# Kernel tuning notes

Hardware: AMD Instinct MI355X
Metric: run time of the kernel (lower is better)

Reference implementation:

```python
import jax, jax.numpy as jnp
import numpy as np

B, S, D, H, HD = 8, 1374, 384, 6, 64
NUM_PATCHES = 1369  # (518 // 14) ** 2
NUM_PREFIX = 5      # 1 cls + 4 registers


def setup_inputs() -> dict:
    key = jax.random.key(0)
    ks = jax.random.split(key, 10)
    init = 0.02  # truncated_normal(0.02) approximated by scaled normal
    x = jax.random.normal(ks[0], (B, S, D), jnp.float32)
    wq = jax.random.truncated_normal(ks[1], -2.0, 2.0, (D, H, HD), jnp.float32) * init
    wk = jax.random.truncated_normal(ks[2], -2.0, 2.0, (D, H, HD), jnp.float32) * init
    wv = jax.random.truncated_normal(ks[3], -2.0, 2.0, (D, H, HD), jnp.float32) * init
    wo = jax.random.truncated_normal(ks[4], -2.0, 2.0, (H, HD, D), jnp.float32) * init
    bq = jnp.zeros((H, HD), jnp.float32)
    bk = jnp.zeros((H, HD), jnp.float32)
    bv = jnp.zeros((H, HD), jnp.float32)
    bo = jnp.zeros((D,), jnp.float32)
    keep_patch_indices = jax.random.randint(ks[5], (B, NUM_PATCHES), 0, NUM_PATCHES).astype(jnp.int64)
    return {"x": x, "wq": wq, "bq": bq, "wk": wk, "bk": bk, "wv": wv, "bv": bv,
            "wo": wo, "bo": bo, "keep_patch_indices": keep_patch_indices, "k_patches": 685}


def reference(x, wq, bq, wk, bk, wv, bv, wo, bo, keep_patch_indices, k_patches):
    # q/k/v projections: DenseGeneral to (heads, head_dim)
    q = jnp.einsum('bsd,dhe->bshe', x, wq) + bq
    k = jnp.einsum('bsd,dhe->bshe', x, wk) + bk
    v = jnp.einsum('bsd,dhe->bshe', x, wv) + bv

    z = jnp.einsum('bqhd,bkhd->bhqk', q / (HD ** 0.5), k)  # [B,H,S,S]
    attn_logits = z  # saved BEFORE masking (used by 'mse' criterion)

    # dynamic scatter mask: patch columns >= k_patches get -inf
    num_selected = keep_patch_indices.shape[1]
    patch_idx = jnp.arange(num_selected)
    indices_to_mask = jnp.where(patch_idx >= k_patches, patch_idx, num_selected) + NUM_PREFIX
    # out-of-bounds indices (== num_selected + NUM_PREFIX) are dropped by JAX scatter semantics
    z = z.at[:, :, :, indices_to_mask].set(-jnp.inf)

    attn_map = jax.nn.softmax(z, axis=-1)
    zo = jnp.einsum('bhqk,bkhd->bqhd', attn_map, v)
    output = jnp.einsum('bqhd,hdo->bqo', zo, wo) + bo  # wo contracts (heads, head_dim)

    # attn_aggregate = ['cls_token','reg_token','patch_token'], zoom_map_criterion='mse'
    am = attn_logits.mean(axis=1)  # mean over heads -> [B,S,S]
    aggs = jnp.stack([
        am[:, 0:1, :].mean(axis=1),      # cls token
        am[:, 1:5, :].mean(axis=1),      # register tokens
        am[:, 5:1374, :].mean(axis=1),   # patch tokens
    ], axis=1)                            # [B,3,S]
    attn_agg = aggs.mean(axis=1)          # [B,S]
    return output, attn_agg
```

## Files before the change

### kernel.cpp

```cpp
#include <hip/hip_runtime.h>
#include <stdint.h>

#define BB 8
#define SS 1374
#define DD 384
#define HH 6
#define HDIM 64
#define MROWS (BB*SS)
#define NPFX 5
#define SPAD 1376

typedef __attribute__((ext_vector_type(8))) short bf16x8;
typedef __attribute__((ext_vector_type(4))) float f32x4;
typedef __attribute__((ext_vector_type(2))) unsigned int u32x2;
typedef __attribute__((ext_vector_type(4))) unsigned int u32x4;
typedef u32x4 __attribute__((aligned(4))) u32x4_u;

__device__ __forceinline__ unsigned short f2bf(float f){
  union { float f; unsigned int u; } v; v.f = f;
  return (unsigned short)((v.u + 0x7FFFu + ((v.u >> 16) & 1u)) >> 16);
}
__device__ __forceinline__ float bf2f(unsigned short b){
  union { float f; unsigned int u; } v; v.u = ((unsigned int)b) << 16; return v.f;
}
__device__ __forceinline__ unsigned int pk_bf16(float a, float b){
#if __has_builtin(__builtin_amdgcn_cvt_pk_bf16_f32)
  typedef __attribute__((ext_vector_type(2))) __bf16 bfv2;
  bfv2 p = __builtin_amdgcn_cvt_pk_bf16_f32(a, b);
  union { bfv2 v; unsigned int u; } c; c.v = p; return c.u;
#else
  return (unsigned int)f2bf(a) | ((unsigned int)f2bf(b) << 16);
#endif
}

__global__ void k_prep_x(const float* __restrict__ x, unsigned short* __restrict__ xb,
                         float* __restrict__ xbar){
  int b = blockIdx.x / 43, ch = blockIdx.x % 43;
  int d = threadIdx.x;
  int s0 = ch*32, s1 = s0 + 32; if (s1 > SS) s1 = SS;
  float acc = 0.f;
  for (int s = s0; s < s1; ++s){
    float v = x[((size_t)b*SS + s)*DD + d];
    float w = (s == 0) ? (1.f/3.f) : (s < 5) ? (1.f/12.f) : (1.f/4107.f);
    acc += w * v;
    xb[((size_t)b*SS + s)*DD + d] = f2bf(v);
  }
  atomicAdd(&xbar[b*DD + d], acc);
}

__global__ void k_conv_w(const float* __restrict__ wq, const float* __restrict__ wk,
                         const float* __restrict__ wv, const float* __restrict__ wo,
                         unsigned short* __restrict__ wbT, unsigned short* __restrict__ woT){
  int i = blockIdx.x*blockDim.x + threadIdx.x;
  if (i < 1152*384){
    int n = i / 384, d = i % 384;
    const float* w = (n < 384) ? wq : (n < 768) ? wk : wv;
    wbT[i] = f2bf(w[(size_t)d*384 + (n % 384)]);
  } else if (i < 1152*384 + 384*384){
    int j = i - 1152*384;
    int n = j / 384, k = j % 384;
    woT[j] = f2bf(wo[(size_t)k*384 + n]);
  }
}

__global__ void k_qbar(const float* __restrict__ xbar, const float* __restrict__ wq,
                       const float* __restrict__ bq, float* __restrict__ qbar){
  __shared__ float xs[DD];
  int b = blockIdx.x, t = threadIdx.x;
  xs[t] = xbar[b*DD + t];
  __syncthreads();
  float acc = bq[t];
  for (int d = 0; d < DD; ++d) acc += xs[d]*wq[(size_t)d*384 + t];
  qbar[b*384 + t] = acc;
}

__global__ void k_agg(const float* __restrict__ qbar, const unsigned short* __restrict__ kg,
                      float* __restrict__ out_agg){
  __shared__ float qs[384];
  int b = blockIdx.x / 6, sb = blockIdx.x % 6;
  int t = threadIdx.x;
  for (int i = t; i < 384; i += 256) qs[i] = qbar[b*384 + i];
  __syncthreads();
  int s = sb*256 + t;
  if (s >= SS) return;
  float acc = 0.f;
  for (int h = 0; h < HH; ++h){
    const unsigned short* kr = kg + (((size_t)(b*HH + h))*SS + s)*64;
    const float* qh = qs + h*64;
    for (int c = 0; c < 8; ++c){
      u32x4 v = *(const u32x4*)(kr + c*8);
      #pragma unroll
      for (int j = 0; j < 4; ++j){
        unsigned int u = v[j];
        acc += qh[c*8 + 2*j]     * bf2f((unsigned short)(u & 0xFFFFu));
        acc += qh[c*8 + 2*j + 1] * bf2f((unsigned short)(u >> 16));
      }
    }
  }
  out_agg[b*SS + s] = acc * (1.f/48.f);
}

template<int MODE>
__global__ __launch_bounds__(256) void k_gemm(
    const unsigned short* __restrict__ A, const unsigned short* __restrict__ Bt,
    const float* __restrict__ b0, const float* __restrict__ b1, const float* __restrict__ b2,
    unsigned short* __restrict__ qg, unsigned short* __restrict__ kgp,
    unsigned short* __restrict__ vt, float* __restrict__ out)
{
  int mt = blockIdx.x % 86, nt = blockIdx.x / 86;
  const int t = threadIdx.x;
  const int w = t >> 6, lane = t & 63, quad = lane >> 4, l16 = lane & 15;
  const int wm = w >> 1, wn = w & 1;
  constexpr int SMEM_SH = (MODE==0) ? 13824 : 17408;
  __shared__ unsigned short smem[SMEM_SH];
  unsigned short* As = smem;
  unsigned short* Bs = smem + 9216;
  f32x4 acc[4][2];
  #pragma unroll
  for (int i=0;i<4;i++){ acc[i][0] = (f32x4){0,0,0,0}; acc[i][1] = (f32x4){0,0,0,0}; }
  const int m0 = mt*128, n0 = nt*64;

  const int ar = t >> 1, akb = (t & 1) * 32;
  int ga = m0 + ar; if (ga > MROWS-1) ga = MROWS-1;
  const unsigned short* ap = A + (size_t)ga*384 + akb;
  const int br = t >> 2, bkb = (t & 3) * 16;
  const unsigned short* bp = Bt + (size_t)(n0 + br)*384 + bkb;

  u32x4 ra[4], rb[2];
  #pragma unroll
  for (int i=0;i<4;i++) ra[i] = *(const u32x4*)(ap + i*8);
  rb[0] = *(const u32x4*)(bp); rb[1] = *(const u32x4*)(bp + 8);

  for (int kc = 0; kc < 6; ++kc){
    __syncthreads();
    #pragma unroll
    for (int i=0;i<4;i++) *(u32x4*)(As + ar*72 + akb + i*8) = ra[i];
    *(u32x4*)(Bs + br*72 + bkb)     = rb[0];
    *(u32x4*)(Bs + br*72 + bkb + 8) = rb[1];
    __syncthreads();
    if (kc + 1 < 6){
      int kn = (kc+1)*64;
      #pragma unroll
      for (int i=0;i<4;i++) ra[i] = *(const u32x4*)(ap + kn + i*8);
      rb[0] = *(const u32x4*)(bp + kn); rb[1] = *(const u32x4*)(bp + kn + 8);
    }
    #pragma unroll
    for (int kh = 0; kh < 2; ++kh){
      bf16x8 af[4], bfr[2];
      #pragma unroll
      for (int rf = 0; rf < 4; ++rf)
        af[rf] = *(const bf16x8*)(As + (wm*64 + rf*16 + l16)*72 + kh*32 + quad*8);
      #pragma unroll
      for (int cf = 0; cf < 2; ++cf)
        bfr[cf] = *(const bf16x8*)(Bs + (wn*32 + cf*16 + l16)*72 + kh*32 + quad*8);
      #pragma unroll
      for (int rf = 0; rf < 4; ++rf)
        #pragma unroll
        for (int cf = 0; cf < 2; ++cf)
          acc[rf][cf] = __builtin_amdgcn_mfma_f32_16x16x32_bf16(af[rf], bfr[cf], acc[rf][cf], 0,0,0);
    }
  }

  const int b0r = m0 / SS, s0r = m0 % SS;
  __syncthreads();
  if (MODE == 1){
    float* CsF = (float*)smem;
    #pragma unroll
    for (int cf = 0; cf < 2; ++cf){
      int e = wn*32 + cf*16 + l16;
      float bias = b0[n0 + e];
      #pragma unroll
      for (int rf = 0; rf < 4; ++rf){
        int rr = wm*64 + rf*16 + quad*4;
        #pragma unroll
        for (int r4 = 0; r4 < 4; ++r4)
          CsF[(rr + r4)*68 + e] = acc[rf][cf][r4] + bias;
      }
    }
    __syncthreads();
    #pragma unroll
    for (int p = 0; p < 8; ++p){
      int r = p*16 + (t >> 4), c = t & 15;
      int rr = m0 + r;
      if (rr < MROWS){
        f32x4 v = *(const f32x4*)(CsF + r*68 + c*4);
        *(f32x4*)(out + (size_t)rr*384 + n0 + c*4) = v;
      }
    }
  } else {
    const int mat = nt / 6, h = nt - mat*6;
    const float* bvp = (mat==0) ? b0 : (mat==1) ? b1 : b2;
    const float vsc = (mat==0) ? 0.125f : 1.f;
    if (mat < 2){
      unsigned short* Cs = As;
      unsigned short* dst = (mat==0) ? qg : kgp;
      #pragma unroll
      for (int cf = 0; cf < 2; ++cf){
        int e = wn*32 + cf*16 + l16;
        float bias = bvp[h*64 + e];
        #pragma unroll
        for (int rf = 0; rf < 4; ++rf){
          int rr = wm*64 + rf*16 + quad*4;
          #pragma unroll
          for (int r4 = 0; r4 < 4; ++r4)
            Cs[(rr + r4)*72 + e] = f2bf((acc[rf][cf][r4] + bias)*vsc);
        }
      }
      __syncthreads();
      #pragma unroll
      for (int p = 0; p < 4; ++p){
        int r = p*32 + (t >> 3), c = t & 7;
        int rr = m0 + r;
        if (rr < MROWS){
          int s = s0r + r, bb = b0r;
          if (s >= SS){ s -= SS; ++bb; }
          u32x4 v = *(const u32x4*)(Cs + r*72 + c*8);
          *(u32x4*)(dst + (((size_t)(bb*HH + h))*SS + s)*64 + c*8) = v;
        }
      }
    } else {
      unsigned short* CsV = As;
      #pragma unroll
      for (int cf = 0; cf < 2; ++cf){
        int e = wn*32 + cf*16 + l16;
        float bias = bvp[h*64 + e];
        #pragma unroll
        for (int rf = 0; rf < 4; ++rf){
          int rr = wm*64 + rf*16 + quad*4;
          #pragma unroll
          for (int p = 0; p < 2; ++p)
            *(unsigned int*)(CsV + e*136 + rr + p*2) =
                pk_bf16(acc[rf][cf][p*2] + bias, acc[rf][cf][p*2+1] + bias);
        }
      }
      __syncthreads();
      const bool nowrap = (s0r + 127 < SS) && (m0 + 127 < MROWS);
      if (nowrap){
        int e = t >> 2;
        unsigned short* vrow = vt + ((size_t)(b0r*HH + h)*64 + e)*SPAD + s0r;
        #pragma unroll
        for (int i = 0; i < 4; ++i){
          int c = (t & 3)*4 + i;
          u32x4 v = *(const u32x4*)(CsV + e*136 + c*8);
          *(u32x4_u*)(vrow + c*8) = v;
        }
      } else {
        for (int idx = t; idx < 64*64; idx += 256){
          int e = idx >> 6, sp = (idx & 63)*2;
          int rr = m0 + sp;
          if (rr < MROWS){
            int s = s0r + sp, bb = b0r;
            if (s >= SS){ s -= SS; ++bb; }
            *(unsigned int*)(vt + ((size_t)(bb*HH + h)*64 + e)*SPAD + s) =
                *(const unsigned int*)(CsV + e*136 + sp);
          }
        }
      }
    }
  }
}

#define KSTR 72
__global__ __launch_bounds__(128) void k_attn(
    const unsigned short* __restrict__ qg, const unsigned short* __restrict__ kg,
    const unsigned short* __restrict__ vt, unsigned short* __restrict__ zo,
    const int* __restrict__ kpat)
{
  const int QB = 43;
  int qb = blockIdx.x % QB, bh = blockIdx.x / QB;
  int t = threadIdx.x, w = t >> 6, lane = t & 63, quad = lane >> 4, l16 = lane & 15;
  int SK = NPFX + kpat[0]; if (SK > SS) SK = SS; if (SK < 1) SK = 1;
  int niter = (SK + 63) >> 6;
  __shared__ unsigned short Ks[64*KSTR];
  __shared__ unsigned short Vs[64*KSTR];
  __shared__ unsigned short Ps[2][16*KSTR];
  unsigned short* Pw = &Ps[w][0];
  int q0 = qb*32 + w*16;
  bf16x8 aq[2];
  {
    int qrow = q0 + l16; if (qrow > SS-1) qrow = SS-1;
    const unsigned short* p = qg + ((size_t)bh*SS + qrow)*64;
    aq[0] = *(const bf16x8*)(p + quad*8);
    aq[1] = *(const bf16x8*)(p + 32 + quad*8);
  }
  f32x4 o[4];
  #pragma unroll
  for (int i=0;i<4;i++) o[i] = (f32x4){0.f,0.f,0.f,0.f};
  float rsum[4] = {0.f,0.f,0.f,0.f};

  const int srow = t >> 1, shalf = (t & 1)*32;
  const unsigned short* kbase = kg + ((size_t)bh*SS)*64;
  const unsigned short* vbase = vt + ((size_t)bh*64)*SPAD;
  u32x4 rk[4], rv[4];
  #pragma unroll
  for (int i=0;i<4;i++){
    rk[i] = *(const u32x4*)(kbase + (size_t)srow*64 + shalf + i*8);
    rv[i] = *(const u32x4*)(vbase + (size_t)srow*SPAD + shalf + i*8);
  }

  for (int it = 0; it < niter; ++it){
    int k0 = it*64;
    __syncthreads();
    #pragma unroll
    for (int i=0;i<4;i++){
      *(u32x4*)(Ks + srow*KSTR + shalf + i*8) = rk[i];
      *(u32x4*)(Vs + srow*KSTR + shalf + i*8) = rv[i];
    }
    __syncthreads();
    if (it + 1 < niter){
      int kn = k0 + 64;
      #pragma unroll
      for (int i=0;i<4;i++){
        rk[i] = *(const u32x4*)(kbase + (size_t)(kn + srow)*64 + shalf + i*8);
        rv[i] = *(const u32x4*)(vbase + (size_t)srow*SPAD + kn + shalf + i*8);
      }
    }
    bool tail = (k0 + 64 > SK);
    #pragma unroll
    for (int ks = 0; ks < 2; ++ks){
      float pp[2][4];
      #pragma unroll
      for (int ns = 0; ns < 2; ++ns){
        f32x4 zf = (f32x4){0.f,0.f,0.f,0.f};
        #pragma unroll
        for (int ec = 0; ec < 2; ++ec){
          bf16x8 bkf = *(const bf16x8*)(Ks + (ks*32 + 2*l16 + ns)*KSTR + ec*32 + quad*8);
          zf = __builtin_amdgcn_mfma_f32_16x16x32_bf16(aq[ec], bkf, zf, 0,0,0);
        }
        bool valid = !tail || (k0 + ks*32 + 2*l16 + ns) < SK;
        #pragma unroll
        for (int rg = 0; rg < 4; ++rg) pp[ns][rg] = valid ? __expf(zf[rg]) : 0.f;
      }
      #pragma unroll
      for (int rg = 0; rg < 4; ++rg){
        rsum[rg] += pp[0][rg] + pp[1][rg];
        *(unsigned int*)(Pw + (quad*4 + rg)*KSTR + ks*32 + 2*l16) =
            pk_bf16(pp[0][rg], pp[1][rg]);
      }
    }
    #pragma unroll
    for (int kc = 0; kc < 2; ++kc){
      bf16x8 ap = *(const bf16x8*)(Pw + l16*KSTR + kc*32 + quad*8);
      #pragma unroll
      for (int nc = 0; nc < 4; ++nc){
        bf16x8 vf = *(const bf16x8*)(Vs + (nc*16 + l16)*KSTR + kc*32 + quad*8);
        o[nc] = __builtin_amdgcn_mfma_f32_16x16x32_bf16(ap, vf, o[nc], 0,0,0);
      }
    }
  }
  int b = bh / HH, h = bh - (bh/HH)*HH;
  #pragma unroll
  for (int rg = 0; rg < 4; ++rg){
    float s = rsum[rg];
    #pragma unroll
    for (int off = 8; off >= 1; off >>= 1) s += __shfl_xor(s, off);
    int q = q0 + quad*4 + rg;
    if (q >= SS) continue;
    float inv = 1.f / s;
    unsigned short* dst = zo + ((size_t)b*SS + q)*384 + h*64;
    #pragma unroll
    for (int nc = 0; nc < 4; ++nc) dst[nc*16 + l16] = f2bf(o[nc][rg]*inv);
  }
}

extern "C" void kernel_launch(void* const* d_in, const int* in_sizes, int n_in,
                              void* d_out, int out_size, void* d_ws, size_t ws_size,
                              hipStream_t stream){
  const float* x  = (const float*)d_in[0];
  const float* wq = (const float*)d_in[1];
  const float* bq = (const float*)d_in[2];
  const float* wk = (const float*)d_in[3];
  const float* bk = (const float*)d_in[4];
  const float* wv = (const float*)d_in[5];
  const float* bv = (const float*)d_in[6];
  const float* wo = (const float*)d_in[7];
  const float* bo = (const float*)d_in[8];
  const int* kpat = (const int*)d_in[10];
  float* out = (float*)d_out;
  float* out_agg = out + (size_t)MROWS*DD;

  char* ws = (char*)d_ws;
  unsigned short* xb  = (unsigned short*)(ws);
  unsigned short* wbT = (unsigned short*)(ws +  8441856);
  unsigned short* woT = (unsigned short*)(ws +  9326592);
  unsigned short* qg  = (unsigned short*)(ws +  9621504);
  unsigned short* kg  = (unsigned short*)(ws + 18063360);
  unsigned short* vt  = (unsigned short*)(ws + 26505216);
  unsigned short* zo  = (unsigned short*)(ws + 34959360);
  float* xbar         = (float*)(ws + 43401216);
  float* qbar         = (float*)(ws + 43413504);
  (void)in_sizes; (void)n_in; (void)out_size; (void)ws_size;

  hipMemsetAsync(xbar, 0, BB*DD*sizeof(float), stream);
  k_prep_x<<<BB*43, DD, 0, stream>>>(x, xb, xbar);
  k_conv_w<<<((1152*384 + 384*384) + 255)/256, 256, 0, stream>>>(wq, wk, wv, wo, wbT, woT);
  k_qbar<<<BB, DD, 0, stream>>>(xbar, wq, bq, qbar);
  k_gemm<0><<<86*18, 256, 0, stream>>>(xb, wbT, bq, bk, bv, qg, kg, vt, nullptr);
  k_attn<<<48*43, 128, 0, stream>>>(qg, kg, vt, zo, kpat);
  k_agg<<<BB*6, 256, 0, stream>>>(qbar, kg, out_agg);
  k_gemm<1><<<86*6, 256, 0, stream>>>(zo, woT, bo, nullptr, nullptr, nullptr, nullptr, nullptr, out);
}
```

Before: 190.5 us.

## Skip dead V projection tiles and load K/V fragments directly in attention

The QKV GEMM now returns early for V-column tiles whose rows lie entirely in key positions that the mask excludes, so it never computes V values attention does not read. The attention kernel doubles the query rows per warp to 32, halving the grid. It drops the shared-memory K/V staging and its barriers, loading MFMA operand fragments straight from global memory with a register prefetch of the next K block. This reduces LDS traffic and synchronisation at the cost of uncoalesced fragment loads and higher register pressure.

```diff
diff --git a/kernel.cpp b/kernel.cpp
--- a/kernel.cpp
+++ b/kernel.cpp
@@ -105,12 +105,22 @@
     const unsigned short* __restrict__ A, const unsigned short* __restrict__ Bt,
     const float* __restrict__ b0, const float* __restrict__ b1, const float* __restrict__ b2,
     unsigned short* __restrict__ qg, unsigned short* __restrict__ kgp,
-    unsigned short* __restrict__ vt, float* __restrict__ out)
+    unsigned short* __restrict__ vt, float* __restrict__ out,
+    const int* __restrict__ kpat)
 {
   int mt = blockIdx.x % 86, nt = blockIdx.x / 86;
   const int t = threadIdx.x;
   const int w = t >> 6, lane = t & 63, quad = lane >> 4, l16 = lane & 15;
   const int wm = w >> 1, wn = w & 1;
+  const int m0 = mt*128, n0 = nt*64;
+
+  if (MODE == 0 && nt >= 12){
+    int s0r_ = m0 % SS;
+    int SKv = NPFX + kpat[0]; if (SKv > SS) SKv = SS; if (SKv < 1) SKv = 1;
+    int lo = (SKv + 63) & ~63;
+    if (s0r_ >= lo && s0r_ + 127 < SS) return;
+  }
+
   constexpr int SMEM_SH = (MODE==0) ? 13824 : 17408;
   __shared__ unsigned short smem[SMEM_SH];
   unsigned short* As = smem;
@@ -118,7 +128,6 @@
   f32x4 acc[4][2];
   #pragma unroll
   for (int i=0;i<4;i++){ acc[i][0] = (f32x4){0,0,0,0}; acc[i][1] = (f32x4){0,0,0,0}; }
-  const int m0 = mt*128, n0 = nt*64;
 
   const int ar = t >> 1, akb = (t & 1) * 32;
   int ga = m0 + ar; if (ga > MROWS-1) ga = MROWS-1;
@@ -260,107 +269,121 @@
   }
 }
 
-#define KSTR 72
+#define PSTR 80
 __global__ __launch_bounds__(128) void k_attn(
     const unsigned short* __restrict__ qg, const unsigned short* __restrict__ kg,
     const unsigned short* __restrict__ vt, unsigned short* __restrict__ zo,
     const int* __restrict__ kpat)
 {
-  const int QB = 43;
-  int qb = blockIdx.x % QB, bh = blockIdx.x / QB;
+  const int NQB = 22;
+  int qb = blockIdx.x % NQB, bh = blockIdx.x / NQB;
   int t = threadIdx.x, w = t >> 6, lane = t & 63, quad = lane >> 4, l16 = lane & 15;
   int SK = NPFX + kpat[0]; if (SK > SS) SK = SS; if (SK < 1) SK = 1;
   int niter = (SK + 63) >> 6;
-  __shared__ unsigned short Ks[64*KSTR];
-  __shared__ unsigned short Vs[64*KSTR];
-  __shared__ unsigned short Ps[2][16*KSTR];
+  __shared__ unsigned short Ps[2][32*PSTR];
   unsigned short* Pw = &Ps[w][0];
-  int q0 = qb*32 + w*16;
-  bf16x8 aq[2];
-  {
-    int qrow = q0 + l16; if (qrow > SS-1) qrow = SS-1;
+  int q0 = qb*64 + w*32;
+
+  bf16x8 aq[2][2];
+  #pragma unroll
+  for (int rt = 0; rt < 2; ++rt){
+    int qrow = q0 + rt*16 + l16; if (qrow > SS-1) qrow = SS-1;
     const unsigned short* p = qg + ((size_t)bh*SS + qrow)*64;
-    aq[0] = *(const bf16x8*)(p + quad*8);
-    aq[1] = *(const bf16x8*)(p + 32 + quad*8);
-  }
-  f32x4 o[4];
-  #pragma unroll
-  for (int i=0;i<4;i++) o[i] = (f32x4){0.f,0.f,0.f,0.f};
-  float rsum[4] = {0.f,0.f,0.f,0.f};
-
-  const int srow = t >> 1, shalf = (t & 1)*32;
+    aq[rt][0] = *(const bf16x8*)(p + quad*8);
+    aq[rt][1] = *(const bf16x8*)(p + 32 + quad*8);
+  }
+  f32x4 o[2][4];
+  float rsum[2][4];
+  #pragma unroll
+  for (int rt=0;rt<2;++rt){
+    #pragma unroll
+    for (int i=0;i<4;i++){ o[rt][i] = (f32x4){0.f,0.f,0.f,0.f}; rsum[rt][i] = 0.f; }
+  }
   const unsigned short* kbase = kg + ((size_t)bh*SS)*64;
   const unsigned short* vbase = vt + ((size_t)bh*64)*SPAD;
-  u32x4 rk[4], rv[4];
-  #pragma unroll
-  for (int i=0;i<4;i++){
-    rk[i] = *(const u32x4*)(kbase + (size_t)srow*64 + shalf + i*8);
-    rv[i] = *(const u32x4*)(vbase + (size_t)srow*SPAD + shalf + i*8);
-  }
+
+  bf16x8 kf[2][2][2];
+  #pragma unroll
+  for (int ks=0; ks<2; ++ks)
+    #pragma unroll
+    for (int ns=0; ns<2; ++ns){
+      const unsigned short* kp = kbase + (size_t)(ks*32 + 2*l16 + ns)*64;
+      kf[ks][ns][0] = *(const bf16x8*)(kp + quad*8);
+      kf[ks][ns][1] = *(const bf16x8*)(kp + 32 + quad*8);
+    }
 
   for (int it = 0; it < niter; ++it){
     int k0 = it*64;
-    __syncthreads();
-    #pragma unroll
-    for (int i=0;i<4;i++){
-      *(u32x4*)(Ks + srow*KSTR + shalf + i*8) = rk[i];
-      *(u32x4*)(Vs + srow*KSTR + shalf + i*8) = rv[i];
-    }
-    __syncthreads();
+    bool tail = (k0 + 64 > SK);
+    bf16x8 vf[2][4];
+    #pragma unroll
+    for (int kc=0;kc<2;++kc)
+      #pragma unroll
+      for (int nc=0;nc<4;++nc)
+        vf[kc][nc] = *(const bf16x8*)(vbase + (size_t)(nc*16 + l16)*SPAD + k0 + kc*32 + quad*8);
+
+    #pragma unroll
+    for (int ks=0;ks<2;++ks){
+      f32x4 zf[2][2];
+      #pragma unroll
+      for (int rt=0;rt<2;++rt)
+        #pragma unroll
+        for (int ns=0;ns<2;++ns){
+          f32x4 z = (f32x4){0.f,0.f,0.f,0.f};
+          z = __builtin_amdgcn_mfma_f32_16x16x32_bf16(aq[rt][0], kf[ks][ns][0], z, 0,0,0);
+          z = __builtin_amdgcn_mfma_f32_16x16x32_bf16(aq[rt][1], kf[ks][ns][1], z, 0,0,0);
+          zf[rt][ns] = z;
+        }
+      bool v0 = !tail || (k0 + ks*32 + 2*l16)     < SK;
+      bool v1 = !tail || (k0 + ks*32 + 2*l16 + 1) < SK;
+      #pragma unroll
+      for (int rt=0;rt<2;++rt){
+        #pragma unroll
+        for (int rg=0;rg<4;++rg){
+          float p0 = v0 ? __expf(zf[rt][0][rg]) : 0.f;
+          float p1 = v1 ? __expf(zf[rt][1][rg]) : 0.f;
+          rsum[rt][rg] += p0 + p1;
+          *(unsigned int*)(Pw + (rt*16 + quad*4 + rg)*PSTR + ks*32 + 2*l16) = pk_bf16(p0, p1);
+        }
+      }
+    }
     if (it + 1 < niter){
       int kn = k0 + 64;
       #pragma unroll
-      for (int i=0;i<4;i++){
-        rk[i] = *(const u32x4*)(kbase + (size_t)(kn + srow)*64 + shalf + i*8);
-        rv[i] = *(const u32x4*)(vbase + (size_t)srow*SPAD + kn + shalf + i*8);
-      }
-    }
-    bool tail = (k0 + 64 > SK);
-    #pragma unroll
-    for (int ks = 0; ks < 2; ++ks){
-      float pp[2][4];
-      #pragma unroll
-      for (int ns = 0; ns < 2; ++ns){
-        f32x4 zf = (f32x4){0.f,0.f,0.f,0.f};
-        #pragma unroll
-        for (int ec = 0; ec < 2; ++ec){
-          bf16x8 bkf = *(const bf16x8*)(Ks + (ks*32 + 2*l16 + ns)*KSTR + ec*32 + quad*8);
-          zf = __builtin_amdgcn_mfma_f32_16x16x32_bf16(aq[ec], bkf, zf, 0,0,0);
-        }
-        bool valid = !tail || (k0 + ks*32 + 2*l16 + ns) < SK;
-        #pragma unroll
-        for (int rg = 0; rg < 4; ++rg) pp[ns][rg] = valid ? __expf(zf[rg]) : 0.f;
-      }
-      #pragma unroll
-      for (int rg = 0; rg < 4; ++rg){
-        rsum[rg] += pp[0][rg] + pp[1][rg];
-        *(unsigned int*)(Pw + (quad*4 + rg)*KSTR + ks*32 + 2*l16) =
-            pk_bf16(pp[0][rg], pp[1][rg]);
-      }
-    }
-    #pragma unroll
-    for (int kc = 0; kc < 2; ++kc){
-      bf16x8 ap = *(const bf16x8*)(Pw + l16*KSTR + kc*32 + quad*8);
-      #pragma unroll
-      for (int nc = 0; nc < 4; ++nc){
-        bf16x8 vf = *(const bf16x8*)(Vs + (nc*16 + l16)*KSTR + kc*32 + quad*8);
-        o[nc] = __builtin_amdgcn_mfma_f32_16x16x32_bf16(ap, vf, o[nc], 0,0,0);
-      }
-    }
-  }
+      for (int ks=0; ks<2; ++ks)
+        #pragma unroll
+        for (int ns=0; ns<2; ++ns){
+          const unsigned short* kp = kbase + (size_t)(kn + ks*32 + 2*l16 + ns)*64;
+          kf[ks][ns][0] = *(const bf16x8*)(kp + quad*8);
+          kf[ks][ns][1] = *(const bf16x8*)(kp + 32 + quad*8);
+        }
+    }
+    #pragma unroll
+    for (int rt=0;rt<2;++rt)
+      #pragma unroll
+      for (int kc=0;kc<2;++kc){
+        bf16x8 ap = *(const bf16x8*)(Pw + (rt*16 + l16)*PSTR + kc*32 + quad*8);
+        #pragma unroll
+        for (int nc=0;nc<4;++nc)
+          o[rt][nc] = __builtin_amdgcn_mfma_f32_16x16x32_bf16(ap, vf[kc][nc], o[rt][nc], 0,0,0);
+      }
+  }
+
   int b = bh / HH, h = bh - (bh/HH)*HH;
   #pragma unroll
-  for (int rg = 0; rg < 4; ++rg){
-    float s = rsum[rg];
-    #pragma unroll
-    for (int off = 8; off >= 1; off >>= 1) s += __shfl_xor(s, off);
-    int q = q0 + quad*4 + rg;
-    if (q >= SS) continue;
-    float inv = 1.f / s;
-    unsigned short* dst = zo + ((size_t)b*SS + q)*384 + h*64;
-    #pragma unroll
-    for (int nc = 0; nc < 4; ++nc) dst[nc*16 + l16] = f2bf(o[nc][rg]*inv);
-  }
+  for (int rt=0;rt<2;++rt)
+    #pragma unroll
+    for (int rg = 0; rg < 4; ++rg){
+      float s = rsum[rt][rg];
+      #pragma unroll
+      for (int off = 8; off >= 1; off >>= 1) s += __shfl_xor(s, off);
+      int q = q0 + rt*16 + quad*4 + rg;
+      if (q >= SS) continue;
+      float inv = 1.f / s;
+      unsigned short* dst = zo + ((size_t)b*SS + q)*384 + h*64;
+      #pragma unroll
+      for (int nc = 0; nc < 4; ++nc) dst[nc*16 + l16] = f2bf(o[rt][nc][rg]*inv);
+    }
 }
 
 extern "C" void kernel_launch(void* const* d_in, const int* in_sizes, int n_in,
@@ -395,8 +418,8 @@
   k_prep_x<<<BB*43, DD, 0, stream>>>(x, xb, xbar);
   k_conv_w<<<((1152*384 + 384*384) + 255)/256, 256, 0, stream>>>(wq, wk, wv, wo, wbT, woT);
   k_qbar<<<BB, DD, 0, stream>>>(xbar, wq, bq, qbar);
-  k_gemm<0><<<86*18, 256, 0, stream>>>(xb, wbT, bq, bk, bv, qg, kg, vt, nullptr);
-  k_attn<<<48*43, 128, 0, stream>>>(qg, kg, vt, zo, kpat);
+  k_gemm<0><<<86*18, 256, 0, stream>>>(xb, wbT, bq, bk, bv, qg, kg, vt, nullptr, kpat);
+  k_attn<<<48*22, 128, 0, stream>>>(qg, kg, vt, zo, kpat);
   k_agg<<<BB*6, 256, 0, stream>>>(qbar, kg, out_agg);
-  k_gemm<1><<<86*6, 256, 0, stream>>>(zo, woT, bo, nullptr, nullptr, nullptr, nullptr, nullptr, out);
-}
+  k_gemm<1><<<86*6, 256, 0, stream>>>(zo, woT, bo, nullptr, nullptr, nullptr, nullptr, nullptr, out, nullptr);
+}
```

Measured after the change: 199.0 us. 4.4% more time.

## Skip unused V projection tiles and double-buffer K/V in larger attention blocks

Applied to the files above, without the earlier changes.

The QKV GEMM now returns early for V-column tiles (nt>=12) whose whole row range lies beyond the unmasked key range, since those V rows are never read by attention. The attention kernel moves to 256-thread blocks covering 64 queries, which halves K/V loads per query, and double-buffers the K/V shared tiles so one barrier per iteration is removed. The early skip depends on the runtime k_patches value and leaves stale V data in the skipped rows. The larger blocks use more shared memory and launch fewer of them.

```diff
diff --git a/kernel.cpp b/kernel.cpp
--- a/kernel.cpp
+++ b/kernel.cpp
@@ -105,12 +105,22 @@
     const unsigned short* __restrict__ A, const unsigned short* __restrict__ Bt,
     const float* __restrict__ b0, const float* __restrict__ b1, const float* __restrict__ b2,
     unsigned short* __restrict__ qg, unsigned short* __restrict__ kgp,
-    unsigned short* __restrict__ vt, float* __restrict__ out)
+    unsigned short* __restrict__ vt, float* __restrict__ out,
+    const int* __restrict__ kpat)
 {
   int mt = blockIdx.x % 86, nt = blockIdx.x / 86;
   const int t = threadIdx.x;
   const int w = t >> 6, lane = t & 63, quad = lane >> 4, l16 = lane & 15;
   const int wm = w >> 1, wn = w & 1;
+  const int m0 = mt*128, n0 = nt*64;
+
+  if (MODE == 0 && nt >= 12){
+    int s0r_ = m0 % SS;
+    int SKv = NPFX + kpat[0]; if (SKv > SS) SKv = SS; if (SKv < 1) SKv = 1;
+    int lo = (SKv + 63) & ~63;
+    if (s0r_ >= lo && s0r_ + 127 < SS) return;
+  }
+
   constexpr int SMEM_SH = (MODE==0) ? 13824 : 17408;
   __shared__ unsigned short smem[SMEM_SH];
   unsigned short* As = smem;
@@ -118,7 +128,6 @@
   f32x4 acc[4][2];
   #pragma unroll
   for (int i=0;i<4;i++){ acc[i][0] = (f32x4){0,0,0,0}; acc[i][1] = (f32x4){0,0,0,0}; }
-  const int m0 = mt*128, n0 = nt*64;
 
   const int ar = t >> 1, akb = (t & 1) * 32;
   int ga = m0 + ar; if (ga > MROWS-1) ga = MROWS-1;
@@ -261,21 +270,22 @@
 }
 
 #define KSTR 72
-__global__ __launch_bounds__(128) void k_attn(
+__global__ __launch_bounds__(256) void k_attn(
     const unsigned short* __restrict__ qg, const unsigned short* __restrict__ kg,
     const unsigned short* __restrict__ vt, unsigned short* __restrict__ zo,
     const int* __restrict__ kpat)
 {
-  const int QB = 43;
-  int qb = blockIdx.x % QB, bh = blockIdx.x / QB;
+  const int NQB = 22;
+  int qb = blockIdx.x % NQB, bh = blockIdx.x / NQB;
   int t = threadIdx.x, w = t >> 6, lane = t & 63, quad = lane >> 4, l16 = lane & 15;
   int SK = NPFX + kpat[0]; if (SK > SS) SK = SS; if (SK < 1) SK = 1;
   int niter = (SK + 63) >> 6;
-  __shared__ unsigned short Ks[64*KSTR];
-  __shared__ unsigned short Vs[64*KSTR];
-  __shared__ unsigned short Ps[2][16*KSTR];
+  __shared__ unsigned short Ks[2][64*KSTR];
+  __shared__ unsigned short Vs[2][64*KSTR];
+  __shared__ unsigned short Ps[4][16*KSTR];
   unsigned short* Pw = &Ps[w][0];
-  int q0 = qb*32 + w*16;
+  int q0 = qb*64 + w*16;
+
   bf16x8 aq[2];
   {
     int qrow = q0 + l16; if (qrow > SS-1) qrow = SS-1;
@@ -284,36 +294,39 @@
     aq[1] = *(const bf16x8*)(p + 32 + quad*8);
   }
   f32x4 o[4];
+  float rsum[4] = {0.f,0.f,0.f,0.f};
   #pragma unroll
   for (int i=0;i<4;i++) o[i] = (f32x4){0.f,0.f,0.f,0.f};
-  float rsum[4] = {0.f,0.f,0.f,0.f};
-
-  const int srow = t >> 1, shalf = (t & 1)*32;
+
+  const int srow = t >> 2, sc = (t & 3) * 16;
   const unsigned short* kbase = kg + ((size_t)bh*SS)*64;
   const unsigned short* vbase = vt + ((size_t)bh*64)*SPAD;
-  u32x4 rk[4], rv[4];
-  #pragma unroll
-  for (int i=0;i<4;i++){
-    rk[i] = *(const u32x4*)(kbase + (size_t)srow*64 + shalf + i*8);
-    rv[i] = *(const u32x4*)(vbase + (size_t)srow*SPAD + shalf + i*8);
+  u32x4 rk[2], rv[2];
+  {
+    int krow = srow; if (krow > SS-1) krow = SS-1;
+    rk[0] = *(const u32x4*)(kbase + (size_t)krow*64 + sc);
+    rk[1] = *(const u32x4*)(kbase + (size_t)krow*64 + sc + 8);
+    rv[0] = *(const u32x4*)(vbase + (size_t)srow*SPAD + sc);
+    rv[1] = *(const u32x4*)(vbase + (size_t)srow*SPAD + sc + 8);
   }
 
   for (int it = 0; it < niter; ++it){
     int k0 = it*64;
-    __syncthreads();
-    #pragma unroll
-    for (int i=0;i<4;i++){
-      *(u32x4*)(Ks + srow*KSTR + shalf + i*8) = rk[i];
-      *(u32x4*)(Vs + srow*KSTR + shalf + i*8) = rv[i];
-    }
+    int cur = it & 1;
+    unsigned short* Ksc = &Ks[cur][0];
+    unsigned short* Vsc = &Vs[cur][0];
+    *(u32x4*)(Ksc + srow*KSTR + sc)     = rk[0];
+    *(u32x4*)(Ksc + srow*KSTR + sc + 8) = rk[1];
+    *(u32x4*)(Vsc + srow*KSTR + sc)     = rv[0];
+    *(u32x4*)(Vsc + srow*KSTR + sc + 8) = rv[1];
     __syncthreads();
     if (it + 1 < niter){
       int kn = k0 + 64;
-      #pragma unroll
-      for (int i=0;i<4;i++){
-        rk[i] = *(const u32x4*)(kbase + (size_t)(kn + srow)*64 + shalf + i*8);
-        rv[i] = *(const u32x4*)(vbase + (size_t)srow*SPAD + kn + shalf + i*8);
-      }
+      int krow = kn + srow; if (krow > SS-1) krow = SS-1;
+      rk[0] = *(const u32x4*)(kbase + (size_t)krow*64 + sc);
+      rk[1] = *(const u32x4*)(kbase + (size_t)krow*64 + sc + 8);
+      rv[0] = *(const u32x4*)(vbase + (size_t)srow*SPAD + kn + sc);
+      rv[1] = *(const u32x4*)(vbase + (size_t)srow*SPAD + kn + sc + 8);
     }
     bool tail = (k0 + 64 > SK);
     #pragma unroll
@@ -324,7 +337,7 @@
         f32x4 zf = (f32x4){0.f,0.f,0.f,0.f};
         #pragma unroll
         for (int ec = 0; ec < 2; ++ec){
-          bf16x8 bkf = *(const bf16x8*)(Ks + (ks*32 + 2*l16 + ns)*KSTR + ec*32 + quad*8);
+          bf16x8 bkf = *(const bf16x8*)(Ksc + (ks*32 + 2*l16 + ns)*KSTR + ec*32 + quad*8);
           zf = __builtin_amdgcn_mfma_f32_16x16x32_bf16(aq[ec], bkf, zf, 0,0,0);
         }
         bool valid = !tail || (k0 + ks*32 + 2*l16 + ns) < SK;
@@ -343,7 +356,7 @@
       bf16x8 ap = *(const bf16x8*)(Pw + l16*KSTR + kc*32 + quad*8);
       #pragma unroll
       for (int nc = 0; nc < 4; ++nc){
-        bf16x8 vf = *(const bf16x8*)(Vs + (nc*16 + l16)*KSTR + kc*32 + quad*8);
+        bf16x8 vf = *(const bf16x8*)(Vsc + (nc*16 + l16)*KSTR + kc*32 + quad*8);
         o[nc] = __builtin_amdgcn_mfma_f32_16x16x32_bf16(ap, vf, o[nc], 0,0,0);
       }
     }
@@ -395,8 +408,8 @@
   k_prep_x<<<BB*43, DD, 0, stream>>>(x, xb, xbar);
   k_conv_w<<<((1152*384 + 384*384) + 255)/256, 256, 0, stream>>>(wq, wk, wv, wo, wbT, woT);
   k_qbar<<<BB, DD, 0, stream>>>(xbar, wq, bq, qbar);
-  k_gemm<0><<<86*18, 256, 0, stream>>>(xb, wbT, bq, bk, bv, qg, kg, vt, nullptr);
-  k_attn<<<48*43, 128, 0, stream>>>(qg, kg, vt, zo, kpat);
+  k_gemm<0><<<86*18, 256, 0, stream>>>(xb, wbT, bq, bk, bv, qg, kg, vt, nullptr, kpat);
+  k_attn<<<48*22, 256, 0, stream>>>(qg, kg, vt, zo, kpat);
   k_agg<<<BB*6, 256, 0, stream>>>(qbar, kg, out_agg);
-  k_gemm<1><<<86*6, 256, 0, stream>>>(zo, woT, bo, nullptr, nullptr, nullptr, nullptr, nullptr, out);
-}
+  k_gemm<1><<<86*6, 256, 0, stream>>>(zo, woT, bo, nullptr, nullptr, nullptr, nullptr, nullptr, out, nullptr);
+}
```

After: 182.9 us. -4.0%, faster.
